# Kernel optimization log

Hardware: AMD Instinct MI355X
Metric: run time of the kernel (lower is better)

The kernel has to match this reference:

```python
import jax, jax.numpy as jnp
import numpy as np

B, I, H, OH = 16384, 256, 256, 64
N_STEPS = 8  # fixed-step dopri5 (adaptive step control replaced by fixed grid for jit)


def setup_inputs() -> dict:
    key = jax.random.key(0)
    ks = jax.random.split(key, 12)
    sH = 1.0 / np.sqrt(H)
    sOH = 1.0 / np.sqrt(OH)
    u = lambda k, shape, s: jax.random.uniform(k, shape, jnp.float32, -s, s)
    return {
        "input": jax.random.normal(ks[0], (B, I), jnp.float32),
        "h_prev": jax.random.normal(ks[1], (B, H), jnp.float32),
        "c_prev": jax.random.normal(ks[2], (B, H), jnp.float32),
        "timespans": jax.random.uniform(ks[3], (B,), jnp.float32, 0.05, 1.0),
        # LSTMCell params (PyTorch layout: gates stacked as [i, f, g, o])
        "W_ih": u(ks[4], (4 * H, I), sH),
        "W_hh": u(ks[5], (4 * H, H), sH),
        "b_ih": u(ks[6], (4 * H,), sH),
        "b_hh": u(ks[7], (4 * H,), sH),
        # ode_func: Linear(H, OH) -> Tanh -> Linear(OH, H)
        "W1": u(ks[8], (OH, H), sH),
        "b1": u(ks[9], (OH,), sH),
        "W2": u(ks[10], (H, OH), sOH),
        "b2": u(ks[11], (H,), sOH),
    }


def reference(input, h_prev, c_prev, timespans, W_ih, W_hh, b_ih, b_hh, W1, b1, W2, b2):
    # --- LSTMCell ---
    gates = input @ W_ih.T + b_ih + h_prev @ W_hh.T + b_hh  # (B, 4H)
    gi, gf, gg, go = jnp.split(gates, 4, axis=-1)
    i = jax.nn.sigmoid(gi)
    f = jax.nn.sigmoid(gf)
    g = jnp.tanh(gg)
    o = jax.nn.sigmoid(go)
    c = f * c_prev + i * g
    h = o * jnp.tanh(c)

    # --- Neural ODE: dy/dt = MLP(y), autonomous, Dormand-Prince RK45 ---
    def ode_f(y):
        return jnp.tanh(y @ W1.T + b1) @ W2.T + b2

    dt = (timespans / N_STEPS)[:, None]  # (B, 1) per-sample step size

    def dopri5_step(y, _):
        k1 = ode_f(y)
        k2 = ode_f(y + dt * (1.0 / 5.0 * k1))
        k3 = ode_f(y + dt * (3.0 / 40.0 * k1 + 9.0 / 40.0 * k2))
        k4 = ode_f(y + dt * (44.0 / 45.0 * k1 - 56.0 / 15.0 * k2 + 32.0 / 9.0 * k3))
        k5 = ode_f(y + dt * (19372.0 / 6561.0 * k1 - 25360.0 / 2187.0 * k2
                             + 64448.0 / 6561.0 * k3 - 212.0 / 729.0 * k4))
        k6 = ode_f(y + dt * (9017.0 / 3168.0 * k1 - 355.0 / 33.0 * k2
                             + 46732.0 / 5247.0 * k3 + 49.0 / 176.0 * k4
                             - 5103.0 / 18656.0 * k5))
        y_next = y + dt * (35.0 / 384.0 * k1 + 500.0 / 1113.0 * k3 + 125.0 / 192.0 * k4
                           - 2187.0 / 6784.0 * k5 + 11.0 / 84.0 * k6)
        return y_next, None

    h_ode, _ = jax.lax.scan(dopri5_step, h, None, length=N_STEPS)
    return h_ode, c
```

## Files before the change

### kernel.cpp

```cpp
#include <hip/hip_runtime.h>
#include <hip/hip_bf16.h>


#define B_N 16384
#define H_N 256

typedef __attribute__((ext_vector_type(8))) short short8;
typedef __attribute__((ext_vector_type(4))) unsigned short u16x4;
typedef __attribute__((ext_vector_type(4))) float f32x4;

__device__ __forceinline__ unsigned short f2bf_s(float x) {
  __hip_bfloat16 h = __float2bfloat16(x);
  return *reinterpret_cast<unsigned short*>(&h);
}

__device__ __forceinline__ short8 pack8f(const float* p) {
  const f32x4 a = *(const f32x4*)p;
  const f32x4 b = *(const f32x4*)(p + 4);
  short8 r;
  r[0] = (short)f2bf_s(a[0]); r[1] = (short)f2bf_s(a[1]);
  r[2] = (short)f2bf_s(a[2]); r[3] = (short)f2bf_s(a[3]);
  r[4] = (short)f2bf_s(b[0]); r[5] = (short)f2bf_s(b[1]);
  r[6] = (short)f2bf_s(b[2]); r[7] = (short)f2bf_s(b[3]);
  return r;
}

__device__ __forceinline__ u16x4 pack4(f32x4 v) {
  u16x4 r;
  r[0] = f2bf_s(v[0]); r[1] = f2bf_s(v[1]);
  r[2] = f2bf_s(v[2]); r[3] = f2bf_s(v[3]);
  return r;
}

__device__ __forceinline__ float fast_sigmoid(float x) {
  return __builtin_amdgcn_rcpf(1.f + __expf(-x));
}
__device__ __forceinline__ float fast_tanh(float x) {
  float e = __expf(2.f * x);
  return 1.f - 2.f * __builtin_amdgcn_rcpf(e + 1.f);
}

__device__ __forceinline__ void gl_lds16(const void* g, void* l) {
  __builtin_amdgcn_global_load_lds(
      (const __attribute__((address_space(1))) void*)g,
      (__attribute__((address_space(3))) void*)l, 16, 0, 0);
}

__global__ __launch_bounds__(256) void prep_kernel(
    const float* __restrict__ Wih, const float* __restrict__ Whh,
    const float* __restrict__ W1, const float* __restrict__ W2,
    const float* __restrict__ b2,
    unsigned short* __restrict__ wsB, unsigned short* __restrict__ wcB,
    float* __restrict__ uF, unsigned short* __restrict__ w1B,
    unsigned short* __restrict__ w2B) {
  const int bx = blockIdx.x;
  if (bx < 256) {
    int idx = bx * 256 + threadIdx.x;
    int n = idx >> 6, c = idx & 63, k = c * 8;
    const float* src = (k < 256) ? (Wih + (size_t)n * 256 + k)
                                 : (Whh + (size_t)n * 256 + (k - 256));
    *(short8*)(wsB + (size_t)n * 512 + k) = pack8f(src);
  } else if (bx < 272) {
    int idx = (bx - 256) * 256 + threadIdx.x;
    int f = idx >> 6, o = idx & 63;
    float a0 = 0.f, a1 = 0.f, a2 = 0.f, a3 = 0.f;
    for (int h = 0; h < 256; h += 4) {
      a0 = fmaf(W1[f * 256 + h],     W2[h * 64 + o],        a0);
      a1 = fmaf(W1[f * 256 + h + 1], W2[(h + 1) * 64 + o],  a1);
      a2 = fmaf(W1[f * 256 + h + 2], W2[(h + 2) * 64 + o],  a2);
      a3 = fmaf(W1[f * 256 + h + 3], W2[(h + 3) * 64 + o],  a3);
    }
    wcB[f * 64 + o] = f2bf_s((a0 + a1) + (a2 + a3));
  } else if (bx == 272) {
    int f = threadIdx.x;
    if (f < 64) {
      float a0 = 0.f, a1 = 0.f, a2 = 0.f, a3 = 0.f;
      for (int h = 0; h < 256; h += 4) {
        a0 = fmaf(W1[f * 256 + h],     b2[h],     a0);
        a1 = fmaf(W1[f * 256 + h + 1], b2[h + 1], a1);
        a2 = fmaf(W1[f * 256 + h + 2], b2[h + 2], a2);
        a3 = fmaf(W1[f * 256 + h + 3], b2[h + 3], a3);
      }
      uF[f] = (a0 + a1) + (a2 + a3);
    }
  } else if (bx < 281) {
    int idx = (bx - 273) * 256 + threadIdx.x;
    *(short8*)(w1B + (size_t)idx * 8) = pack8f(W1 + (size_t)idx * 8);
  } else {
    int idx = (bx - 281) * 256 + threadIdx.x;
    *(short8*)(w2B + (size_t)idx * 8) = pack8f(W2 + (size_t)idx * 8);
  }
}

__global__ __launch_bounds__(512, 4) void lstm_kernel(
    const float* __restrict__ x, const float* __restrict__ hp,
    const float* __restrict__ cp, const unsigned short* __restrict__ wsB,
    const float* __restrict__ bih, const float* __restrict__ bhh,
    float* __restrict__ out) {
  __shared__ __align__(16) float As2[2][128 * 32];
  __shared__ __align__(16) unsigned short Bs2[2][256 * 32];

  const int tid = threadIdx.x;
  const int lane = tid & 63;
  const int wv = tid >> 6;
  const int rg = wv >> 1;
  const int cg = wv & 1;
  const int s = lane & 15, q = lane >> 4;
  const int mb = blockIdx.x * 128;
  const int hb = blockIdx.y * 64;

  f32x4 acc[2][8];
#pragma unroll
  for (int mt = 0; mt < 2; ++mt)
#pragma unroll
    for (int tn = 0; tn < 8; ++tn) acc[mt][tn] = (f32x4){0.f, 0.f, 0.f, 0.f};

  const int c16a = wv * 2;
  const int rowA0 = c16a * 8 + (lane >> 3);
  const int gcA = (lane & 7) ^ (rowA0 & 7);
  const int rowB0 = c16a * 16 + (lane >> 2);
  const int rowB1 = rowB0 + 16;
  const int gcB0 = (lane & 3) ^ ((rowB0 >> 1) & 3);
  const int gcB1 = (lane & 3) ^ ((rowB1 >> 1) & 3);
  const int grB0 = (rowB0 >> 6) * 256 + hb + (rowB0 & 63);
  const int grB1 = (rowB1 >> 6) * 256 + hb + (rowB1 & 63);

  auto STAGE = [&](int buf, int kt) {
    const float* srcA = (kt < 8) ? x : hp;
    const int kl = (kt * 32) & 255;
    gl_lds16(srcA + (size_t)(mb + rowA0) * 256 + kl + gcA * 4,
             (char*)As2[buf] + c16a * 1024);
    gl_lds16(srcA + (size_t)(mb + rowA0 + 8) * 256 + kl + gcA * 4,
             (char*)As2[buf] + (c16a + 1) * 1024);
    gl_lds16(wsB + (size_t)grB0 * 512 + kt * 32 + gcB0 * 8,
             (char*)Bs2[buf] + c16a * 1024);
    gl_lds16(wsB + (size_t)grB1 * 512 + kt * 32 + gcB1 * 8,
             (char*)Bs2[buf] + (c16a + 1) * 1024);
  };

  STAGE(0, 0);
  __syncthreads();

  for (int kt = 0; kt < 16; ++kt) {
    const int buf = kt & 1;
    if (kt < 15) STAGE(buf ^ 1, kt + 1);

    short8 af[2];
#pragma unroll
    for (int mt = 0; mt < 2; ++mt) {
      const int ar = rg * 32 + mt * 16 + s;
      const char* ap = (const char*)As2[buf] + ar * 128;
      float tmp[8];
      *(f32x4*)tmp = *(const f32x4*)(ap + (((q * 2) ^ (ar & 7)) << 4));
      *(f32x4*)(tmp + 4) = *(const f32x4*)(ap + (((q * 2 + 1) ^ (ar & 7)) << 4));
      af[mt] = pack8f(tmp);
    }
    const char* bp = (const char*)Bs2[buf];
#pragma unroll
    for (int tn = 0; tn < 8; ++tn) {
      const int t = (tn >> 1) * 64 + cg * 32 + (tn & 1) * 16 + s;
      short8 bfr = *(const short8*)(bp + t * 64 + ((q ^ ((t >> 1) & 3)) << 4));
      acc[0][tn] = __builtin_amdgcn_mfma_f32_16x16x32_bf16(af[0], bfr, acc[0][tn], 0, 0, 0);
      acc[1][tn] = __builtin_amdgcn_mfma_f32_16x16x32_bf16(af[1], bfr, acc[1][tn], 0, 0, 0);
    }
    __syncthreads();
  }

#pragma unroll
  for (int mt = 0; mt < 2; ++mt)
#pragma unroll
    for (int ntl = 0; ntl < 2; ++ntl)
#pragma unroll
      for (int r = 0; r < 4; ++r) {
        int sample = mb + rg * 32 + mt * 16 + q * 4 + r;
        int h = hb + cg * 32 + ntl * 16 + s;
        float gi = acc[mt][0 + ntl][r] + bih[h] + bhh[h];
        float gf = acc[mt][2 + ntl][r] + bih[256 + h] + bhh[256 + h];
        float gg = acc[mt][4 + ntl][r] + bih[512 + h] + bhh[512 + h];
        float go = acc[mt][6 + ntl][r] + bih[768 + h] + bhh[768 + h];
        float iv = fast_sigmoid(gi), fv = fast_sigmoid(gf);
        float gv = fast_tanh(gg), ov = fast_sigmoid(go);
        float c = fv * cp[(size_t)sample * 256 + h] + iv * gv;
        float hv = ov * fast_tanh(c);
        out[(size_t)B_N * H_N + (size_t)sample * 256 + h] = c;
        out[(size_t)sample * 256 + h] = hv;
      }
}

__global__ __launch_bounds__(64) void ode_kernel(
    float* __restrict__ out, const float* __restrict__ ts,
    const unsigned short* __restrict__ wcB, const float* __restrict__ uF,
    const unsigned short* __restrict__ w1B, const unsigned short* __restrict__ w2B,
    const float* __restrict__ b1, const float* __restrict__ b2) {
  __shared__ __align__(16) unsigned short zbuf[16 * 80];
  char* zb = (char*)zbuf;

  const int lane = threadIdx.x;
  const int s = lane & 15, q = lane >> 4;
  const int bb = blockIdx.x * 16;
  const int wb = s * 160;

  short8 wcf[4][2];
#pragma unroll
  for (int i = 0; i < 4; ++i)
#pragma unroll
    for (int kt = 0; kt < 2; ++kt)
      wcf[i][kt] = *(const short8*)(wcB + (size_t)(i * 16 + s) * 64 + kt * 32 + q * 8);
  f32x4 b1v[4], u4[4];
#pragma unroll
  for (int i = 0; i < 4; ++i) {
    b1v[i] = *(const f32x4*)(b1 + i * 16 + q * 4);
    u4[i] = *(const f32x4*)(uF + i * 16 + q * 4);
  }
  const float dt = ts[bb + s] * 0.125f;

  f32x4 G[4];
#pragma unroll
  for (int i = 0; i < 4; ++i) G[i] = (f32x4){0.f, 0.f, 0.f, 0.f};
#pragma unroll
  for (int kt = 0; kt < 8; ++kt) {
    short8 yf = pack8f(out + (size_t)(bb + s) * 256 + kt * 32 + q * 8);
#pragma unroll
    for (int i = 0; i < 4; ++i) {
      short8 w1f = *(const short8*)(w1B + (size_t)(i * 16 + s) * 256 + kt * 32 + q * 8);
      G[i] = __builtin_amdgcn_mfma_f32_16x16x32_bf16(w1f, yf, G[i], 0, 0, 0);
    }
  }

  auto exch = [&](const f32x4 (&v)[4]) {
#pragma unroll
    for (int i = 0; i < 4; ++i)
      *(u16x4*)(zb + wb + i * 32 + q * 8) = pack4(v[i]);
    asm volatile("s_waitcnt lgkmcnt(0)" ::: "memory");
    __builtin_amdgcn_sched_barrier(0);
  };
  auto wcmm = [&](f32x4 (&o)[4]) {
    short8 zf0 = *(const short8*)(zb + wb + q * 16);
    short8 zf1 = *(const short8*)(zb + wb + 64 + q * 16);
#pragma unroll
    for (int i = 0; i < 4; ++i) {
      f32x4 a = (f32x4){0.f, 0.f, 0.f, 0.f};
      a = __builtin_amdgcn_mfma_f32_16x16x32_bf16(wcf[i][0], zf0, a, 0, 0, 0);
      a = __builtin_amdgcn_mfma_f32_16x16x32_bf16(wcf[i][1], zf1, a, 0, 0, 0);
      o[i] = a;
    }
  };
  auto stage = [&](const f32x4 (&zc)[4], float cj, f32x4 (&zo)[4]) {
    exch(zc);
    f32x4 o[4];
    wcmm(o);
#pragma unroll
    for (int i = 0; i < 4; ++i)
#pragma unroll
      for (int r = 0; r < 4; ++r)
        zo[i][r] =
            fast_tanh(fmaf(dt, fmaf(cj, u4[i][r], o[i][r]), G[i][r]) + b1v[i][r]);
  };

  const float A31 = 3.f / 40.f, A32 = 9.f / 40.f;
  const float A41 = 44.f / 45.f, A42 = -56.f / 15.f, A43 = 32.f / 9.f;
  const float A51 = 19372.f / 6561.f, A52 = -25360.f / 2187.f,
              A53 = 64448.f / 6561.f, A54 = -212.f / 729.f;
  const float A61 = 9017.f / 3168.f, A62 = -355.f / 33.f, A63 = 46732.f / 5247.f,
              A64 = 49.f / 176.f, A65 = -5103.f / 18656.f;
  const float C1 = 35.f / 384.f, C3 = 500.f / 1113.f, C4 = 125.f / 192.f,
              C5 = -2187.f / 6784.f, C6 = 11.f / 84.f;

  f32x4 SC[4];
#pragma unroll
  for (int i = 0; i < 4; ++i) SC[i] = (f32x4){0.f, 0.f, 0.f, 0.f};
  f32x4 z1[4], z2[4], z3[4], z4[4], z5[4], zc[4];

  for (int st = 0; st < 8; ++st) {
#pragma unroll
    for (int i = 0; i < 4; ++i)
#pragma unroll
      for (int r = 0; r < 4; ++r) z1[i][r] = fast_tanh(G[i][r] + b1v[i][r]);

#pragma unroll
    for (int i = 0; i < 4; ++i) zc[i] = 0.2f * z1[i];
    stage(zc, 0.2f, z2);
#pragma unroll
    for (int i = 0; i < 4; ++i) zc[i] = A31 * z1[i] + A32 * z2[i];
    stage(zc, 0.3f, z3);
#pragma unroll
    for (int i = 0; i < 4; ++i) zc[i] = A41 * z1[i] + A42 * z2[i] + A43 * z3[i];
    stage(zc, 0.8f, z4);
#pragma unroll
    for (int i = 0; i < 4; ++i)
      zc[i] = A51 * z1[i] + A52 * z2[i] + A53 * z3[i] + A54 * z4[i];
    stage(zc, 8.f / 9.f, z5);
#pragma unroll
    for (int i = 0; i < 4; ++i)
      zc[i] = A61 * z1[i] + A62 * z2[i] + A63 * z3[i] + A64 * z4[i] + A65 * z5[i];
    exch(zc);
    {
      f32x4 o[4];
      wcmm(o);
#pragma unroll
      for (int i = 0; i < 4; ++i)
#pragma unroll
        for (int r = 0; r < 4; ++r) {
          float z6v =
              fast_tanh(fmaf(dt, fmaf(1.0f, u4[i][r], o[i][r]), G[i][r]) + b1v[i][r]);
          zc[i][r] = C1 * z1[i][r] + C3 * z3[i][r] + C4 * z4[i][r] +
                     C5 * z5[i][r] + C6 * z6v;
        }
    }
    exch(zc);
    {
      f32x4 o6[4];
      wcmm(o6);
#pragma unroll
      for (int i = 0; i < 4; ++i) {
        SC[i] += zc[i];
#pragma unroll
        for (int r = 0; r < 4; ++r)
          G[i][r] = fmaf(dt, u4[i][r] + o6[i][r], G[i][r]);
      }
    }
  }

  exch(SC);
  {
    short8 zf0 = *(const short8*)(zb + wb + q * 16);
    short8 zf1 = *(const short8*)(zb + wb + 64 + q * 16);
#pragma unroll
    for (int ft = 0; ft < 16; ++ft) {
      short8 w2a = *(const short8*)(w2B + (size_t)(ft * 16 + s) * 64 + q * 8);
      short8 w2b = *(const short8*)(w2B + (size_t)(ft * 16 + s) * 64 + 32 + q * 8);
      f32x4 a = (f32x4){0.f, 0.f, 0.f, 0.f};
      a = __builtin_amdgcn_mfma_f32_16x16x32_bf16(w2a, zf0, a, 0, 0, 0);
      a = __builtin_amdgcn_mfma_f32_16x16x32_bf16(w2b, zf1, a, 0, 0, 0);
      f32x4 y0 = *(const f32x4*)(out + (size_t)(bb + s) * 256 + ft * 16 + q * 4);
      f32x4 b2v = *(const f32x4*)(b2 + ft * 16 + q * 4);
#pragma unroll
      for (int r = 0; r < 4; ++r)
        y0[r] = fmaf(dt, fmaf(8.f, b2v[r], a[r]), y0[r]);
      *(f32x4*)(out + (size_t)(bb + s) * 256 + ft * 16 + q * 4) = y0;
    }
  }
}

extern "C" void kernel_launch(void* const* d_in, const int* in_sizes, int n_in,
                              void* d_out, int out_size, void* d_ws, size_t ws_size,
                              hipStream_t stream) {
  const float* x   = (const float*)d_in[0];
  const float* hp  = (const float*)d_in[1];
  const float* cp  = (const float*)d_in[2];
  const float* ts  = (const float*)d_in[3];
  const float* Wih = (const float*)d_in[4];
  const float* Whh = (const float*)d_in[5];
  const float* bih = (const float*)d_in[6];
  const float* bhh = (const float*)d_in[7];
  const float* W1  = (const float*)d_in[8];
  const float* b1  = (const float*)d_in[9];
  const float* W2  = (const float*)d_in[10];
  const float* b2  = (const float*)d_in[11];
  float* out = (float*)d_out;

  unsigned short* wsB = (unsigned short*)d_ws;
  unsigned short* wcB = (unsigned short*)((char*)d_ws + 1048576);
  float* uF = (float*)((char*)d_ws + 1048576 + 8192);
  unsigned short* w1B = (unsigned short*)((char*)d_ws + 1048576 + 16384);
  unsigned short* w2B = (unsigned short*)((char*)d_ws + 1048576 + 49152);

  prep_kernel<<<289, 256, 0, stream>>>(Wih, Whh, W1, W2, b2, wsB, wcB, uF, w1B, w2B);
  lstm_kernel<<<dim3(128, 4), 512, 0, stream>>>(x, hp, cp, wsB, bih, bhh, out);
  ode_kernel<<<1024, 64, 0, stream>>>(out, ts, wcB, uF, w1B, w2B, b1, b2);
}
```

Before: 84.11 us.

## Permute hidden-feature rows so MFMA outputs feed next MFMA without LDS exchange

Reorders the 64 ODE hidden features assigned to each MFMA output tile (in W1, Wc, b1 and u) so that the accumulator layout of one 16x16x32 MFMA lines up with the B-operand layout the next MFMA expects. Each stage's intermediate can then be packed straight from registers into bf16 operands. This drops the LDS write, the waitcnt and the sched barrier on every RK stage, which sit on the serial critical path of a one-wave block. The permutation has to match exactly across all weight and bias loads, or results will be wrong.

```diff
diff --git a/kernel.cpp b/kernel.cpp
--- a/kernel.cpp
+++ b/kernel.cpp
@@ -25,10 +25,12 @@
   return r;
 }
 
-__device__ __forceinline__ u16x4 pack4(f32x4 v) {
-  u16x4 r;
-  r[0] = f2bf_s(v[0]); r[1] = f2bf_s(v[1]);
-  r[2] = f2bf_s(v[2]); r[3] = f2bf_s(v[3]);
+__device__ __forceinline__ short8 pack8v(f32x4 a, f32x4 b) {
+  short8 r;
+  r[0] = (short)f2bf_s(a[0]); r[1] = (short)f2bf_s(a[1]);
+  r[2] = (short)f2bf_s(a[2]); r[3] = (short)f2bf_s(a[3]);
+  r[4] = (short)f2bf_s(b[0]); r[5] = (short)f2bf_s(b[1]);
+  r[6] = (short)f2bf_s(b[2]); r[7] = (short)f2bf_s(b[3]);
   return r;
 }
 
@@ -192,25 +194,28 @@
     const unsigned short* __restrict__ wcB, const float* __restrict__ uF,
     const unsigned short* __restrict__ w1B, const unsigned short* __restrict__ w2B,
     const float* __restrict__ b1, const float* __restrict__ b2) {
-  __shared__ __align__(16) unsigned short zbuf[16 * 80];
-  char* zb = (char*)zbuf;
-
   const int lane = threadIdx.x;
   const int s = lane & 15, q = lane >> 4;
   const int bb = blockIdx.x * 16;
-  const int wb = s * 160;
+
+  auto grow = [&](int i) {
+    return (i >> 1) * 32 + ((s >> 2) * 8) + (i & 1) * 4 + (s & 3);
+  };
+  auto fbase = [&](int i) { return (i >> 1) * 32 + q * 8 + (i & 1) * 4; };
 
   short8 wcf[4][2];
 #pragma unroll
-  for (int i = 0; i < 4; ++i)
+  for (int i = 0; i < 4; ++i) {
+    const int gr = grow(i);
 #pragma unroll
     for (int kt = 0; kt < 2; ++kt)
-      wcf[i][kt] = *(const short8*)(wcB + (size_t)(i * 16 + s) * 64 + kt * 32 + q * 8);
+      wcf[i][kt] = *(const short8*)(wcB + (size_t)gr * 64 + kt * 32 + q * 8);
+  }
   f32x4 b1v[4], u4[4];
 #pragma unroll
   for (int i = 0; i < 4; ++i) {
-    b1v[i] = *(const f32x4*)(b1 + i * 16 + q * 4);
-    u4[i] = *(const f32x4*)(uF + i * 16 + q * 4);
+    b1v[i] = *(const f32x4*)(b1 + fbase(i));
+    u4[i] = *(const f32x4*)(uF + fbase(i));
   }
   const float dt = ts[bb + s] * 0.125f;
 
@@ -222,21 +227,15 @@
     short8 yf = pack8f(out + (size_t)(bb + s) * 256 + kt * 32 + q * 8);
 #pragma unroll
     for (int i = 0; i < 4; ++i) {
-      short8 w1f = *(const short8*)(w1B + (size_t)(i * 16 + s) * 256 + kt * 32 + q * 8);
+      short8 w1f =
+          *(const short8*)(w1B + (size_t)grow(i) * 256 + kt * 32 + q * 8);
       G[i] = __builtin_amdgcn_mfma_f32_16x16x32_bf16(w1f, yf, G[i], 0, 0, 0);
     }
   }
 
-  auto exch = [&](const f32x4 (&v)[4]) {
-#pragma unroll
-    for (int i = 0; i < 4; ++i)
-      *(u16x4*)(zb + wb + i * 32 + q * 8) = pack4(v[i]);
-    asm volatile("s_waitcnt lgkmcnt(0)" ::: "memory");
-    __builtin_amdgcn_sched_barrier(0);
-  };
-  auto wcmm = [&](f32x4 (&o)[4]) {
-    short8 zf0 = *(const short8*)(zb + wb + q * 16);
-    short8 zf1 = *(const short8*)(zb + wb + 64 + q * 16);
+  auto wcmm = [&](const f32x4 (&zc)[4], f32x4 (&o)[4]) {
+    short8 zf0 = pack8v(zc[0], zc[1]);
+    short8 zf1 = pack8v(zc[2], zc[3]);
 #pragma unroll
     for (int i = 0; i < 4; ++i) {
       f32x4 a = (f32x4){0.f, 0.f, 0.f, 0.f};
@@ -246,9 +245,8 @@
     }
   };
   auto stage = [&](const f32x4 (&zc)[4], float cj, f32x4 (&zo)[4]) {
-    exch(zc);
     f32x4 o[4];
-    wcmm(o);
+    wcmm(zc, o);
 #pragma unroll
     for (int i = 0; i < 4; ++i)
 #pragma unroll
@@ -293,24 +291,22 @@
 #pragma unroll
     for (int i = 0; i < 4; ++i)
       zc[i] = A61 * z1[i] + A62 * z2[i] + A63 * z3[i] + A64 * z4[i] + A65 * z5[i];
-    exch(zc);
     {
       f32x4 o[4];
-      wcmm(o);
+      wcmm(zc, o);
 #pragma unroll
       for (int i = 0; i < 4; ++i)
 #pragma unroll
         for (int r = 0; r < 4; ++r) {
           float z6v =
-              fast_tanh(fmaf(dt, fmaf(1.0f, u4[i][r], o[i][r]), G[i][r]) + b1v[i][r]);
+              fast_tanh(fmaf(dt, u4[i][r] + o[i][r], G[i][r]) + b1v[i][r]);
           zc[i][r] = C1 * z1[i][r] + C3 * z3[i][r] + C4 * z4[i][r] +
                      C5 * z5[i][r] + C6 * z6v;
         }
     }
-    exch(zc);
     {
       f32x4 o6[4];
-      wcmm(o6);
+      wcmm(zc, o6);
 #pragma unroll
       for (int i = 0; i < 4; ++i) {
         SC[i] += zc[i];
@@ -321,17 +317,16 @@
     }
   }
 
-  exch(SC);
   {
-    short8 zf0 = *(const short8*)(zb + wb + q * 16);
-    short8 zf1 = *(const short8*)(zb + wb + 64 + q * 16);
+    short8 sf0 = pack8v(SC[0], SC[1]);
+    short8 sf1 = pack8v(SC[2], SC[3]);
 #pragma unroll
     for (int ft = 0; ft < 16; ++ft) {
       short8 w2a = *(const short8*)(w2B + (size_t)(ft * 16 + s) * 64 + q * 8);
       short8 w2b = *(const short8*)(w2B + (size_t)(ft * 16 + s) * 64 + 32 + q * 8);
       f32x4 a = (f32x4){0.f, 0.f, 0.f, 0.f};
-      a = __builtin_amdgcn_mfma_f32_16x16x32_bf16(w2a, zf0, a, 0, 0, 0);
-      a = __builtin_amdgcn_mfma_f32_16x16x32_bf16(w2b, zf1, a, 0, 0, 0);
+      a = __builtin_amdgcn_mfma_f32_16x16x32_bf16(w2a, sf0, a, 0, 0, 0);
+      a = __builtin_amdgcn_mfma_f32_16x16x32_bf16(w2b, sf1, a, 0, 0, 0);
       f32x4 y0 = *(const f32x4*)(out + (size_t)(bb + s) * 256 + ft * 16 + q * 4);
       f32x4 b2v = *(const f32x4*)(b2 + ft * 16 + q * 4);
 #pragma unroll
```

Result: faster. 80.73 us (-4.0%).
